# Performance work log

Hardware: AMD Instinct MI355X
Metric: run time of the kernel (lower is better)

Reference implementation:

```python
import jax, jax.numpy as jnp
import numpy as np

B, C_IN, H, W = 4, 128, 32, 128   # W must equal out_channels (fc_out acts on last dim)
C_OUT, NUM_HEADS = 128, 2
BN_EPS = 1e-5


def setup_inputs() -> dict:
    key = jax.random.key(0)
    ks = jax.random.split(key, 14)
    s = 0.05  # small init scale for weights
    d = {
        "x": jax.random.normal(ks[0], (B, C_IN, H, W), jnp.float32),
        "wq": jax.random.normal(ks[1], (C_OUT, C_IN), jnp.float32) * s,
        "bq": jax.random.normal(ks[2], (C_OUT,), jnp.float32) * s,
        "wk": jax.random.normal(ks[3], (C_OUT, C_IN), jnp.float32) * s,
        "bk": jax.random.normal(ks[4], (C_OUT,), jnp.float32) * s,
        "wv": jax.random.normal(ks[5], (C_OUT, C_IN), jnp.float32) * s,
        "bv": jax.random.normal(ks[6], (C_OUT,), jnp.float32) * s,
        "fc_w": jax.random.normal(ks[7], (C_OUT, C_OUT), jnp.float32) * s,
        "fc_b": jax.random.normal(ks[8], (C_OUT,), jnp.float32) * s,
        "bn_gamma": jnp.ones((C_OUT,), jnp.float32),
        "bn_beta": jnp.zeros((C_OUT,), jnp.float32),
        "bn_mean": jax.random.normal(ks[9], (C_OUT,), jnp.float32) * 0.1,
        "bn_var": jax.random.uniform(ks[10], (C_OUT,), jnp.float32, 0.5, 1.5),
        "prelu_a": jnp.full((1,), 0.25, jnp.float32),
    }
    return d


def reference(x, wq, bq, wk, bk, wv, bv, fc_w, fc_b,
              bn_gamma, bn_beta, bn_mean, bn_var, prelu_a):
    b, c_in, h, w = x.shape
    c_out = wq.shape[0]
    nh = NUM_HEADS
    dk = c_out // nh
    L = h * w
    xf = x.reshape(b, c_in, L)                                # (B, Cin, L)
    # 1x1 convs == per-token linear projections
    q = jnp.einsum('oi,bil->bol', wq, xf) + bq[:, None]       # (B, Cout, L)
    k = jnp.einsum('oi,bil->bol', wk, xf) + bk[:, None]
    v = jnp.einsum('oi,bil->bol', wv, xf) + bv[:, None]
    Q = q.reshape(b, nh, dk, L)                               # (B, h, d_k, L)
    K = k.reshape(b, nh, dk, L)
    V = v.reshape(b, nh, dk, L)
    # scaled dot-product attention over the L = H*W tokens
    scores = jnp.einsum('bhdl,bhdm->bhlm', Q, K) / jnp.sqrt(jnp.float32(dk))
    attn = jax.nn.softmax(scores, axis=-1)                    # (B, h, L, L)
    out = jnp.einsum('bhlm,bhdm->bhdl', attn, V)              # (B, h, d_k, L)
    out = out.reshape(b, c_out, h, w)                         # (B, Cout, H, W)
    # fc_out: torch Linear on the LAST dim (W == Cout)
    y = jnp.einsum('bchw,ow->bcho', out, fc_w) + fc_b         # (B, Cout, H, W)
    # BatchNorm2d (eval mode: running stats) over channel dim
    inv = jax.lax.rsqrt(bn_var + BN_EPS)
    y = (y - bn_mean[None, :, None, None]) * (inv * bn_gamma)[None, :, None, None] \
        + bn_beta[None, :, None, None]
    # PReLU (single shared slope); dropout is identity in eval
    y = jnp.where(y > 0, y, prelu_a[0] * y)
    return y
```

## Files before the change

### kernel.cpp

```cpp
#include <hip/hip_runtime.h>

typedef _Float16 f16x8 __attribute__((ext_vector_type(8)));
typedef _Float16 f16x4t __attribute__((ext_vector_type(4)));
typedef __fp16 h16x2 __attribute__((ext_vector_type(2)));
typedef float f32x4 __attribute__((ext_vector_type(4)));
typedef float f32x16 __attribute__((ext_vector_type(16)));
typedef unsigned int uint2v __attribute__((ext_vector_type(2)));

#define L_SZ 4096

__device__ __forceinline__ unsigned short f2h(float f) {
    _Float16 h = (_Float16)f;
    return __builtin_bit_cast(unsigned short, h);
}
__device__ __forceinline__ unsigned int pk2(float a, float b) {
    h16x2 p = __builtin_amdgcn_cvt_pkrtz(a, b);
    return __builtin_bit_cast(unsigned int, p);
}
__device__ __forceinline__ float fexp2(float x) {
#if __has_builtin(__builtin_amdgcn_exp2f)
    return __builtin_amdgcn_exp2f(x);
#else
    return exp2f(x);
#endif
}
__device__ __forceinline__ float frcp(float x) {
#if __has_builtin(__builtin_amdgcn_rcpf)
    return __builtin_amdgcn_rcpf(x);
#else
    return 1.0f / x;
#endif
}

#define SLOT(row, ci) ((((ci) * 64) + ((row) & 32) + (((row) & 31) ^ (ci))) * 8)

__global__ __launch_bounds__(256, 3) void qkv_kernel(
    const float* __restrict__ x,
    const float* __restrict__ wq, const float* __restrict__ wk,
    const float* __restrict__ wv,
    const float* __restrict__ bq, const float* __restrict__ bk,
    const float* __restrict__ bv,
    unsigned short* __restrict__ Qp, unsigned short* __restrict__ Kp,
    unsigned short* __restrict__ Vp)
{
    int raw = blockIdx.x;
    int v = (raw & 7) * 96 + (raw >> 3);
    int tile = v / 3;
    int p = v - tile * 3;
    int bidx = tile >> 6;
    int l0 = (tile & 63) * 64;
    int tid = threadIdx.x;
    int wave = tid >> 6, lane = tid & 63;
    int c = lane & 15, qd = lane >> 4;

    __shared__ __align__(16) unsigned short Ws[128 * 128];
    __shared__ __align__(16) unsigned short Sc[9216];

    const float* wsrc = (p == 0) ? wq : (p == 1 ? wk : wv);
    #pragma unroll
    for (int t = 0; t < 32; ++t) {
        int e2 = tid + t * 256;
        float2 wv2 = *(const float2*)&wsrc[e2 * 2];
        int e = e2 * 2;
        int o = e >> 7, ci = (e & 127) >> 3, j = e & 7;
        *(unsigned int*)&Ws[o * 128 + ((ci ^ (o & 15)) * 8) + j] = pk2(wv2.x, wv2.y);
    }

    unsigned short* Xs = Sc;
    #pragma unroll
    for (int it = 0; it < 8; ++it) {
        int i  = (tid >> 4) + 16 * it;
        int l4 = (tid & 15) * 4;
        const float4 vx = *(const float4*)&x[(bidx * 128 + i) * L_SZ + l0 + l4];
        float vv[4] = {vx.x, vx.y, vx.z, vx.w};
        int ci = i >> 3;
        #pragma unroll
        for (int u = 0; u < 4; ++u) {
            int l = l4 + u;
            Xs[l * 128 + ((ci ^ (l & 15)) * 8) + (i & 7)] = f2h(vv[u]);
        }
    }
    __syncthreads();

    f16x8 afrag[4];
    #pragma unroll
    for (int kc = 0; kc < 4; ++kc) {
        int l = wave * 16 + c;
        int ci = kc * 4 + qd;
        afrag[kc] = *(const f16x8*)&Xs[l * 128 + ((ci ^ (l & 15)) * 8)];
    }
    __syncthreads();

    f32x4 acc[8];
    #pragma unroll
    for (int nt = 0; nt < 8; ++nt) acc[nt] = (f32x4){0.f, 0.f, 0.f, 0.f};

    #pragma unroll
    for (int kc = 0; kc < 4; ++kc) {
        #pragma unroll
        for (int nt = 0; nt < 8; ++nt) {
            int o = nt * 16 + c;
            f16x8 bfrag = *(const f16x8*)&Ws[o * 128 + (((kc * 4 + qd) ^ c) * 8)];
            acc[nt] = __builtin_amdgcn_mfma_f32_16x16x32_f16(afrag[kc], bfrag, acc[nt], 0, 0, 0);
        }
    }

    const float s_q = 0.18033688011f;
    if (p == 0) {
        #pragma unroll
        for (int nt = 0; nt < 8; ++nt) {
            int o = nt * 16 + c;
            int h = o >> 6, d = o & 63;
            #pragma unroll
            for (int r = 0; r < 4; ++r) {
                int l = l0 + wave * 16 + qd * 4 + r;
                Qp[((bidx * 2 + h) * L_SZ + l) * 64 + d] = f2h((acc[nt][r] + bq[o]) * s_q);
            }
        }
    } else if (p == 1) {
        #pragma unroll
        for (int nt = 0; nt < 8; ++nt) {
            int o = nt * 16 + c;
            int h = o >> 6, d = o & 63;
            #pragma unroll
            for (int r = 0; r < 4; ++r) {
                int l = l0 + wave * 16 + qd * 4 + r;
                Kp[((bidx * 2 + h) * L_SZ + l) * 64 + d] = f2h(acc[nt][r] + bk[o]);
            }
        }
    } else {
        unsigned short* Vt = Sc;
        #pragma unroll
        for (int nt = 0; nt < 8; ++nt) {
            int o = nt * 16 + c;
            #pragma unroll
            for (int r = 0; r < 4; ++r) {
                int ll = wave * 16 + qd * 4 + r;
                Vt[o * 72 + ll] = f2h(acc[nt][r] + bv[o]);
            }
        }
        __syncthreads();
        #pragma unroll
        for (int t = 0; t < 2; ++t) {
            int u = tid + t * 256;
            int row = u >> 2;
            int lc = (u & 3) * 16;
            uint4 a0 = *(const uint4*)&Vt[row * 72 + lc];
            uint4 a1 = *(const uint4*)&Vt[row * 72 + lc + 8];
            *(uint4*)&Vp[(size_t)(bidx * 128 + row) * L_SZ + l0 + lc] = a0;
            *(uint4*)&Vp[(size_t)(bidx * 128 + row) * L_SZ + l0 + lc + 8] = a1;
        }
    }
}

__global__ __launch_bounds__(256, 4) void attn_kernel(
    const unsigned short* __restrict__ Qp, const unsigned short* __restrict__ Kp,
    const unsigned short* __restrict__ Vp,
    unsigned short* __restrict__ Opart, float* __restrict__ Mpart, float* __restrict__ Lpart)
{
    int raw = blockIdx.x;
    int blk = (raw & 7) * 128 + (raw >> 3);
    int lt = blk & 31;
    int bh = (blk >> 5) & 7;
    int sp = blk >> 8;
    int l0 = lt * 128;
    int tid = threadIdx.x;
    int wave = tid >> 6, lane = tid & 63;
    int ln = lane & 31, hi = lane >> 5;
    int b = bh >> 1, h = bh & 1;

    __shared__ __align__(16) unsigned short Ks[2][4096];
    __shared__ __align__(16) unsigned short Vs[2][4096];

    const unsigned short* Qb = Qp + (size_t)bh * L_SZ * 64;
    const unsigned short* Kb = Kp + (size_t)bh * L_SZ * 64;
    const unsigned short* Vb = Vp + ((size_t)b * 128 + h * 64) * L_SZ;

    int lq = l0 + wave * 32 + ln;
    f16x8 qf[4];
    #pragma unroll
    for (int kc = 0; kc < 4; ++kc)
        qf[kc] = *(const f16x8*)&Qb[(size_t)lq * 64 + kc * 16 + hi * 8];

    float m_st = -1e30f, lsum = 0.f;
    f32x16 acc0 = {}, acc1 = {};

    int urow = tid >> 3, uci = tid & 7;
    int mglob = sp * 1024;

    uint4 kreg[2][2], vreg[2][2];

#define LOADT(s, t) do {                                                      \
        int m0_ = mglob + (t) * 64;                                           \
        kreg[s][0] = *(const uint4*)&Kb[(size_t)(m0_ + urow) * 64 + uci * 8]; \
        kreg[s][1] = *(const uint4*)&Kb[(size_t)(m0_ + urow + 32) * 64 + uci * 8]; \
        vreg[s][0] = *(const uint4*)&Vb[(size_t)urow * L_SZ + m0_ + uci * 8]; \
        vreg[s][1] = *(const uint4*)&Vb[(size_t)(urow + 32) * L_SZ + m0_ + uci * 8]; \
    } while (0)
#define STORET(s, buf) do {                                                   \
        *(uint4*)&Ks[buf][SLOT(urow, uci)]      = kreg[s][0];                 \
        *(uint4*)&Ks[buf][SLOT(urow + 32, uci)] = kreg[s][1];                 \
        *(uint4*)&Vs[buf][SLOT(urow, uci)]      = vreg[s][0];                 \
        *(uint4*)&Vs[buf][SLOT(urow + 32, uci)] = vreg[s][1];                 \
    } while (0)

    LOADT(0, 0);
    STORET(0, 0);
    LOADT(1, 1);

    #pragma unroll 2
    for (int it = 0; it < 16; ++it) {
        int cur = it & 1;
        __syncthreads();
        if (it < 14) {
            LOADT(it & 1, it + 2);
        }

        __builtin_amdgcn_s_setprio(1);
        f32x16 s0 = {}, s1 = {};
        #pragma unroll
        for (int kc = 0; kc < 4; ++kc) {
            int cd = kc * 2 + hi;
            f16x8 k0 = *(const f16x8*)&Ks[cur][SLOT(ln, cd)];
            f16x8 k1 = *(const f16x8*)&Ks[cur][SLOT(32 + ln, cd)];
            s0 = __builtin_amdgcn_mfma_f32_32x32x16_f16(k0, qf[kc], s0, 0, 0, 0);
            s1 = __builtin_amdgcn_mfma_f32_32x32x16_f16(k1, qf[kc], s1, 0, 0, 0);
        }

        float t[8];
        #pragma unroll
        for (int r = 0; r < 8; ++r)
            t[r] = fmaxf(fmaxf(s0[r], s0[r + 8]), s1[r]);
        #pragma unroll
        for (int r = 0; r < 4; ++r)
            t[r] = fmaxf(fmaxf(t[r], t[r + 4]), s1[8 + r]);
        float m01 = fmaxf(fmaxf(t[0], t[1]), s1[12]);
        float m23 = fmaxf(fmaxf(t[2], t[3]), s1[13]);
        float mx = fmaxf(fmaxf(m01, m23), fmaxf(s1[14], s1[15]));
        mx = fmaxf(mx, __shfl_xor(mx, 32));

        if (!__all(mx <= m_st + 8.0f)) {
            float mnew = fmaxf(m_st, mx);
            float alpha = fexp2(m_st - mnew);
            m_st = mnew;
            lsum *= alpha;
            #pragma unroll
            for (int r = 0; r < 16; ++r) { acc0[r] *= alpha; acc1[r] *= alpha; }
        }
        float rs0 = 0.f, rs1 = 0.f, rs2 = 0.f, rs3 = 0.f;
        #pragma unroll
        for (int r = 0; r < 4; ++r) {
            float p0 = fexp2(s0[r]      - m_st); s0[r]      = p0; rs0 += p0;
            float p1 = fexp2(s0[r + 4]  - m_st); s0[r + 4]  = p1; rs1 += p1;
            float p2 = fexp2(s0[r + 8]  - m_st); s0[r + 8]  = p2; rs2 += p2;
            float p3 = fexp2(s0[r + 12] - m_st); s0[r + 12] = p3; rs3 += p3;
        }
        #pragma unroll
        for (int r = 0; r < 4; ++r) {
            float p0 = fexp2(s1[r]      - m_st); s1[r]      = p0; rs0 += p0;
            float p1 = fexp2(s1[r + 4]  - m_st); s1[r + 4]  = p1; rs1 += p1;
            float p2 = fexp2(s1[r + 8]  - m_st); s1[r + 8]  = p2; rs2 += p2;
            float p3 = fexp2(s1[r + 12] - m_st); s1[r + 12] = p3; rs3 += p3;
        }
        lsum += (rs0 + rs1) + (rs2 + rs3);

        #pragma unroll
        for (int kc = 0; kc < 4; ++kc) {
            unsigned int a0, a1, a2, a3;
            if (kc == 0) {
                a0 = pk2(s0[0], s0[1]);  a1 = pk2(s0[2], s0[3]);
                a2 = pk2(s0[4], s0[5]);  a3 = pk2(s0[6], s0[7]);
            } else if (kc == 1) {
                a0 = pk2(s0[8], s0[9]);  a1 = pk2(s0[10], s0[11]);
                a2 = pk2(s0[12], s0[13]); a3 = pk2(s0[14], s0[15]);
            } else if (kc == 2) {
                a0 = pk2(s1[0], s1[1]);  a1 = pk2(s1[2], s1[3]);
                a2 = pk2(s1[4], s1[5]);  a3 = pk2(s1[6], s1[7]);
            } else {
                a0 = pk2(s1[8], s1[9]);  a1 = pk2(s1[10], s1[11]);
                a2 = pk2(s1[12], s1[13]); a3 = pk2(s1[14], s1[15]);
            }
            uint2v r02 = __builtin_amdgcn_permlane32_swap(a0, a2, false, false);
            uint2v r13 = __builtin_amdgcn_permlane32_swap(a1, a3, false, false);
            uint4 pw; pw.x = r02[0]; pw.y = r13[0]; pw.z = r02[1]; pw.w = r13[1];
            f16x8 pf = __builtin_bit_cast(f16x8, pw);
            int cd = kc * 2 + hi;
            f16x8 v0 = *(const f16x8*)&Vs[cur][SLOT(ln, cd)];
            f16x8 v1 = *(const f16x8*)&Vs[cur][SLOT(32 + ln, cd)];
            acc0 = __builtin_amdgcn_mfma_f32_32x32x16_f16(v0, pf, acc0, 0, 0, 0);
            acc1 = __builtin_amdgcn_mfma_f32_32x32x16_f16(v1, pf, acc1, 0, 0, 0);
        }
        __builtin_amdgcn_s_setprio(0);

        if (it < 15) {
            STORET((it + 1) & 1, cur ^ 1);
        }
    }
#undef LOADT
#undef STORET

    float l_tot = lsum + __shfl_xor(lsum, 32);
    unsigned short* Ow = Opart + (size_t)(sp * 8 + bh) * 64 * 4096;
    #pragma unroll
    for (int r = 0; r < 16; ++r) {
        int d0 = (r & 3) + 8 * (r >> 2) + 4 * hi;
        Ow[(size_t)d0 * 4096 + lq] = f2h(acc0[r]);
        Ow[(size_t)(32 + d0) * 4096 + lq] = f2h(acc1[r]);
    }
    if (hi == 0) {
        Mpart[(sp * 8 + bh) * 4096 + lq] = m_st;
        Lpart[(sp * 8 + bh) * 4096 + lq] = l_tot;
    }
}

__global__ __launch_bounds__(256, 2) void fc_kernel(
    const unsigned short* __restrict__ Opart, const float* __restrict__ Mp,
    const float* __restrict__ Lp, const float* __restrict__ fcw_f,
    const float* __restrict__ fc_b, const float* __restrict__ bn_g,
    const float* __restrict__ bn_b, const float* __restrict__ bn_m,
    const float* __restrict__ bn_v, const float* __restrict__ prelu_a,
    float* __restrict__ out)
{
    int raw = blockIdx.x;
    int blk = (raw & 7) * 64 + (raw >> 3);
    int r0 = blk * 32;
    int tid = threadIdx.x;
    int c0 = blk & 127;
    int bh = blk >> 6;
    int d = c0 & 63;

    int wave = tid >> 6, lane = tid & 63;
    int c = lane & 15, qd = lane >> 4;
    int rw = r0 + (wave >> 1) * 16;
    int o0 = (wave & 1) * 64;
    int hh = (rw + c) & 31;

    __shared__ __align__(16) unsigned short Fw[128 * 128];
    __shared__ __align__(16) unsigned short SclU[4096 * 4];

    uint4 ovr[4][4];
    #pragma unroll
    for (int kc = 0; kc < 4; ++kc) {
        int w0 = kc * 32 + qd * 8;
        #pragma unroll
        for (int s = 0; s < 4; ++s)
            ovr[kc][s] = *(const uint4*)&Opart[(size_t)(s * 8 + bh) * 262144 + (size_t)d * 4096 + hh * 128 + w0];
    }

    #pragma unroll
    for (int t = 0; t < 16; ++t) {
        int l = tid + t * 256;
        float m0 = Mp[(0 * 8 + bh) * 4096 + l], m1 = Mp[(1 * 8 + bh) * 4096 + l];
        float m2 = Mp[(2 * 8 + bh) * 4096 + l], m3 = Mp[(3 * 8 + bh) * 4096 + l];
        float mx = fmaxf(fmaxf(m0, m1), fmaxf(m2, m3));
        float a0 = fexp2(m0 - mx), a1 = fexp2(m1 - mx);
        float a2 = fexp2(m2 - mx), a3 = fexp2(m3 - mx);
        float den = a0 * Lp[(0 * 8 + bh) * 4096 + l] + a1 * Lp[(1 * 8 + bh) * 4096 + l]
                  + a2 * Lp[(2 * 8 + bh) * 4096 + l] + a3 * Lp[(3 * 8 + bh) * 4096 + l];
        float inv = frcp(den);
        int hl = l >> 7, ww = l & 127;
        int slot = hl * 128 + ((ww + hl) & 127);
        uint2 sc;
        sc.x = pk2(a0 * inv, a1 * inv);
        sc.y = pk2(a2 * inv, a3 * inv);
        *(uint2*)&SclU[slot * 4] = sc;
    }
    #pragma unroll
    for (int t = 0; t < 32; ++t) {
        int e2 = tid + t * 256;
        float2 v = *(const float2*)&fcw_f[e2 * 2];
        int e = e2 * 2;
        int o = e >> 7, ci = (e & 127) >> 3, j = e & 7;
        *(unsigned int*)&Fw[o * 128 + ((ci ^ (o & 15)) * 8) + j] = pk2(v.x, v.y);
    }
    __syncthreads();

    f16x8 af[4];
    #pragma unroll
    for (int kc = 0; kc < 4; ++kc) {
        int w0 = kc * 32 + qd * 8;
        f16x8 ov0 = __builtin_bit_cast(f16x8, ovr[kc][0]);
        f16x8 ov1 = __builtin_bit_cast(f16x8, ovr[kc][1]);
        f16x8 ov2 = __builtin_bit_cast(f16x8, ovr[kc][2]);
        f16x8 ov3 = __builtin_bit_cast(f16x8, ovr[kc][3]);
        #pragma unroll
        for (int j = 0; j < 8; ++j) {
            int slot = hh * 128 + ((w0 + j + hh) & 127);
            f16x4t sc = *(const f16x4t*)&SclU[slot * 4];
            float v = (float)ov0[j] * (float)sc[0] + (float)ov1[j] * (float)sc[1]
                    + (float)ov2[j] * (float)sc[2] + (float)ov3[j] * (float)sc[3];
            af[kc][j] = (_Float16)v;
        }
    }

    f32x4 acc[4];
    #pragma unroll
    for (int nt = 0; nt < 4; ++nt) acc[nt] = (f32x4){0.f, 0.f, 0.f, 0.f};
    #pragma unroll
    for (int kc = 0; kc < 4; ++kc) {
        #pragma unroll
        for (int nt = 0; nt < 4; ++nt) {
            int o = o0 + nt * 16 + c;
            f16x8 bf = *(const f16x8*)&Fw[o * 128 + (((kc * 4 + qd) ^ c) * 8)];
            acc[nt] = __builtin_amdgcn_mfma_f32_16x16x32_f16(af[kc], bf, acc[nt], 0, 0, 0);
        }
    }

    float pa = prelu_a[0];
    float g  = bn_g[c0] * rsqrtf(bn_v[c0] + 1e-5f);
    float mn = bn_m[c0], bt = bn_b[c0];
    #pragma unroll
    for (int r = 0; r < 4; ++r) {
        int orow = rw + qd * 4 + r;
        #pragma unroll
        for (int nt = 0; nt < 4; ++nt) {
            int o = o0 + nt * 16 + c;
            float y = (acc[nt][r] + fc_b[o] - mn) * g + bt;
            y = y > 0.f ? y : pa * y;
            out[(size_t)orow * 128 + o] = y;
        }
    }
}

extern "C" void kernel_launch(void* const* d_in, const int* in_sizes, int n_in,
                              void* d_out, int out_size, void* d_ws, size_t ws_size,
                              hipStream_t stream) {
    const float* x     = (const float*)d_in[0];
    const float* wq    = (const float*)d_in[1];
    const float* bq    = (const float*)d_in[2];
    const float* wk    = (const float*)d_in[3];
    const float* bk    = (const float*)d_in[4];
    const float* wv    = (const float*)d_in[5];
    const float* bv    = (const float*)d_in[6];
    const float* fcw_f = (const float*)d_in[7];
    const float* fcb   = (const float*)d_in[8];
    const float* bn_g  = (const float*)d_in[9];
    const float* bn_b  = (const float*)d_in[10];
    const float* bn_m  = (const float*)d_in[11];
    const float* bn_v  = (const float*)d_in[12];
    const float* pa    = (const float*)d_in[13];
    float* out = (float*)d_out;

    unsigned short* Qp  = (unsigned short*)d_ws;
    unsigned short* Kp  = Qp + 8 * L_SZ * 64;
    unsigned short* Vp  = Kp + 8 * L_SZ * 64;
    unsigned short* Opart = Vp + 8 * L_SZ * 64;
    float* Mpart = (float*)(Opart + 4 * 8 * 64 * L_SZ);
    float* Lpart = Mpart + 4 * 8 * L_SZ;

    hipLaunchKernelGGL(qkv_kernel,  dim3(768),  dim3(256), 0, stream,
                       x, wq, wk, wv, bq, bk, bv, Qp, Kp, Vp);
    hipLaunchKernelGGL(attn_kernel, dim3(1024), dim3(256), 0, stream,
                       Qp, Kp, Vp, Opart, Mpart, Lpart);
    hipLaunchKernelGGL(fc_kernel,   dim3(512),  dim3(256), 0, stream,
                       Opart, Mpart, Lpart, fcw_f, fcb, bn_g, bn_b, bn_m, bn_v, pa, out);
}
```

Measured before the change: 188.5 us.

## Stage K/V tiles into LDS with direct global_load_lds async copies

The attention kernel previously staged K and V tiles by loading into registers and then writing swizzled 16-byte chunks into shared memory. It now uses global_load_lds 16-byte async copies: each wave writes a contiguous LDS slot and reads the matching swizzled global row, so the existing SLOT layout is kept. This removes the register staging and the explicit ds_write pass, and should free VGPRs. The trade-offs are a shorter prefetch distance (one tile instead of two) and correctness that depends on the barrier waiting for the async LDS writes.

```diff
diff --git a/kernel.cpp b/kernel.cpp
--- a/kernel.cpp
+++ b/kernel.cpp
@@ -30,6 +30,11 @@
 #else
     return 1.0f / x;
 #endif
+}
+__device__ __forceinline__ void async16(unsigned short* lds, const unsigned short* g) {
+    __builtin_amdgcn_global_load_lds(
+        (const __attribute__((address_space(1))) unsigned int*)g,
+        (__attribute__((address_space(3))) unsigned int*)lds, 16, 0, 0);
 }
 
 #define SLOT(row, ci) ((((ci) * 64) + ((row) & 32) + (((row) & 31) ^ (ci))) * 8)
@@ -185,36 +190,25 @@
     float m_st = -1e30f, lsum = 0.f;
     f32x16 acc0 = {}, acc1 = {};
 
-    int urow = tid >> 3, uci = tid & 7;
     int mglob = sp * 1024;
-
-    uint4 kreg[2][2], vreg[2][2];
-
-#define LOADT(s, t) do {                                                      \
-        int m0_ = mglob + (t) * 64;                                           \
-        kreg[s][0] = *(const uint4*)&Kb[(size_t)(m0_ + urow) * 64 + uci * 8]; \
-        kreg[s][1] = *(const uint4*)&Kb[(size_t)(m0_ + urow + 32) * 64 + uci * 8]; \
-        vreg[s][0] = *(const uint4*)&Vb[(size_t)urow * L_SZ + m0_ + uci * 8]; \
-        vreg[s][1] = *(const uint4*)&Vb[(size_t)(urow + 32) * L_SZ + m0_ + uci * 8]; \
+    int ci0 = wave, ci1 = 4 + wave;
+    int r0_ = (lane & 32) | ((lane & 31) ^ ci0);
+    int r1_ = (lane & 32) | ((lane & 31) ^ ci1);
+
+#define STAGE(t, buf) do {                                                        \
+        int m0_ = mglob + (t) * 64;                                               \
+        async16(&Ks[buf][(wave * 64) * 8],       &Kb[(size_t)(m0_ + r0_) * 64 + ci0 * 8]); \
+        async16(&Ks[buf][(256 + wave * 64) * 8], &Kb[(size_t)(m0_ + r1_) * 64 + ci1 * 8]); \
+        async16(&Vs[buf][(wave * 64) * 8],       &Vb[(size_t)r0_ * L_SZ + m0_ + ci0 * 8]); \
+        async16(&Vs[buf][(256 + wave * 64) * 8], &Vb[(size_t)r1_ * L_SZ + m0_ + ci1 * 8]); \
     } while (0)
-#define STORET(s, buf) do {                                                   \
-        *(uint4*)&Ks[buf][SLOT(urow, uci)]      = kreg[s][0];                 \
-        *(uint4*)&Ks[buf][SLOT(urow + 32, uci)] = kreg[s][1];                 \
-        *(uint4*)&Vs[buf][SLOT(urow, uci)]      = vreg[s][0];                 \
-        *(uint4*)&Vs[buf][SLOT(urow + 32, uci)] = vreg[s][1];                 \
-    } while (0)
-
-    LOADT(0, 0);
-    STORET(0, 0);
-    LOADT(1, 1);
-
-    #pragma unroll 2
+
+    STAGE(0, 0);
+
     for (int it = 0; it < 16; ++it) {
         int cur = it & 1;
         __syncthreads();
-        if (it < 14) {
-            LOADT(it & 1, it + 2);
-        }
+        if (it < 15) STAGE(it + 1, cur ^ 1);
 
         __builtin_amdgcn_s_setprio(1);
         f32x16 s0 = {}, s1 = {};
@@ -291,13 +285,8 @@
             acc1 = __builtin_amdgcn_mfma_f32_32x32x16_f16(v1, pf, acc1, 0, 0, 0);
         }
         __builtin_amdgcn_s_setprio(0);
-
-        if (it < 15) {
-            STORET((it + 1) & 1, cur ^ 1);
-        }
-    }
-#undef LOADT
-#undef STORET
+    }
+#undef STAGE
 
     float l_tot = lsum + __shfl_xor(lsum, 32);
     unsigned short* Ow = Opart + (size_t)(sp * 8 + bh) * 64 * 4096;
```

Result: faster. 158.5 us, median of 2 (-16.0%).
